# Optimization experiments

Measured on AMD Instinct MI355X. Metric: run time of the kernel, lower is better.

## Reference

```python
import jax, jax.numpy as jnp
import numpy as np

N = 50000      # nodes
E = 800000     # edges (before self loops)
D = 128        # input_dim == hidden_dim == out_channels
H = 1          # heads
L = 3          # layers
SLOPE = 0.2    # GATv2 leaky_relu negative slope


def setup_inputs() -> dict:
    key = jax.random.key(0)
    ks = jax.random.split(key, 9)
    x = jax.random.normal(ks[0], (N, D), dtype=jnp.float32)
    edge_index = jax.random.randint(ks[1], (2, E), 0, N, dtype=jnp.int32)
    s = 1.0 / np.sqrt(D).astype(np.float32)
    # stacked per-layer GATv2Conv params (all layers are D -> H*D here)
    Wl = jax.random.normal(ks[2], (L, D, H * D), dtype=jnp.float32) * s   # lin_l weights
    bl = jnp.zeros((L, H * D), dtype=jnp.float32)
    Wr = jax.random.normal(ks[3], (L, D, H * D), dtype=jnp.float32) * s   # lin_r weights
    br = jnp.zeros((L, H * D), dtype=jnp.float32)
    att = jax.random.normal(ks[4], (L, H, D), dtype=jnp.float32) * s      # attention vector
    bias = jnp.zeros((L, H * D), dtype=jnp.float32)                       # conv output bias
    return {"x": x, "edge_index": edge_index, "Wl": Wl, "bl": bl,
            "Wr": Wr, "br": br, "att": att, "bias": bias}


def reference(x, edge_index, Wl, bl, Wr, br, att, bias):
    # add self loops (PyG GATv2Conv default)
    loops = jnp.arange(N, dtype=edge_index.dtype)
    src = jnp.concatenate([edge_index[0], loops])  # [E+N] message sources j
    dst = jnp.concatenate([edge_index[1], loops])  # [E+N] message targets i

    h = x
    for l in range(L):
        xl = (h @ Wl[l] + bl[l]).reshape(N, H, D)   # source transform
        xr = (h @ Wr[l] + br[l]).reshape(N, H, D)   # target transform
        # edge-wise GATv2 score: att . leaky_relu(xl_j + xr_i)
        e = jax.nn.leaky_relu(xl[src] + xr[dst], SLOPE)      # [E+N, H, D]
        score = jnp.einsum('ehd,hd->eh', e, att[l])          # [E+N, H]
        # segment softmax over incoming edges of each dst node
        m = jax.ops.segment_max(score, dst, num_segments=N)  # [N, H]
        p = jnp.exp(score - m[dst])
        denom = jax.ops.segment_sum(p, dst, num_segments=N)
        alpha = p / (denom[dst] + 1e-16)                     # [E+N, H]
        # weighted scatter-aggregate of source features
        msg = xl[src] * alpha[:, :, None]                    # [E+N, H, D]
        h = jax.ops.segment_sum(msg, dst, num_segments=N).reshape(N, H * D) + bias[l]
        h = jax.nn.relu(h)
    return jax.nn.log_softmax(h, axis=1)
```

## Files before the change

kernel.cpp:

```cpp
#include <hip/hip_runtime.h>
#include <cstdint>
#include <cstddef>

#define N_NODES 50000
#define N_EDGES 800000
#define ET (N_EDGES + N_NODES)
#define D 128
#define NLAYERS 3
#define SLOPE 0.2f
#define NB_SCAN ((N_NODES + 1023) / 1024)

typedef __bf16 bf16x8 __attribute__((ext_vector_type(8)));
typedef float  f32x4  __attribute__((ext_vector_type(4)));
typedef float  f32x2  __attribute__((ext_vector_type(2)));

__device__ __forceinline__ unsigned short f2bf_rne(float v) {
    unsigned u = __float_as_uint(v);
    u += 0x7fffu + ((u >> 16) & 1u);
    return (unsigned short)(u >> 16);
}
__device__ __forceinline__ float bf2f(unsigned short h) {
    return __uint_as_float(((unsigned)h) << 16);
}
__device__ __forceinline__ f32x2 unpack_bf2(unsigned u) {
    f32x2 r;
    r.x = __uint_as_float(u << 16);
    r.y = __uint_as_float(u & 0xffff0000u);
    return r;
}

__global__ void prep_kernel(const float* __restrict__ x,
                            const float* __restrict__ Wl,
                            const float* __restrict__ Wr,
                            const int* __restrict__ dstp,
                            unsigned short* __restrict__ hhi,
                            unsigned short* __restrict__ hlo,
                            unsigned short* __restrict__ wlh,
                            unsigned short* __restrict__ wll,
                            unsigned short* __restrict__ wrh,
                            int* __restrict__ deg)
{
    int idx = blockIdx.x * blockDim.x + threadIdx.x;
    if (idx < (N_NODES * D) / 4) {
        float4 v = ((const float4*)x)[idx];
        unsigned short h0 = f2bf_rne(v.x), h1 = f2bf_rne(v.y);
        unsigned short h2 = f2bf_rne(v.z), h3 = f2bf_rne(v.w);
        unsigned short l0 = f2bf_rne(v.x - bf2f(h0)), l1 = f2bf_rne(v.y - bf2f(h1));
        unsigned short l2 = f2bf_rne(v.z - bf2f(h2)), l3 = f2bf_rne(v.w - bf2f(h3));
        uint2 hw, lw;
        hw.x = (unsigned)h0 | ((unsigned)h1 << 16);
        hw.y = (unsigned)h2 | ((unsigned)h3 << 16);
        lw.x = (unsigned)l0 | ((unsigned)l1 << 16);
        lw.y = (unsigned)l2 | ((unsigned)l3 << 16);
        ((uint2*)hhi)[idx] = hw;
        ((uint2*)hlo)[idx] = lw;
    }
    if (idx < NLAYERS * D * D) {
        int l   = idx / (D * D);
        int rem = idx - l * D * D;
        int kk  = rem / D;
        int nn  = rem - kk * D;
        int tp  = l * D * D + nn * D + kk;
        float v = Wl[idx];
        unsigned short h = f2bf_rne(v);
        wlh[tp] = h;
        wll[tp] = f2bf_rne(v - bf2f(h));
        wrh[tp] = f2bf_rne(Wr[idx]);
    }
    if (idx < ET) {
        int dt = (idx < N_EDGES) ? dstp[idx] : idx - N_EDGES;
        atomicAdd(deg + dt, 1);
    }
}

__global__ void scan1_kernel(const int* __restrict__ deg,
                             int* __restrict__ incl, int* __restrict__ bsum)
{
    __shared__ int tmp[1024];
    int tid = threadIdx.x;
    int i = blockIdx.x * 1024 + tid;
    int v = (i < N_NODES) ? deg[i] : 0;
    tmp[tid] = v;
    __syncthreads();
    #pragma unroll
    for (int o = 1; o < 1024; o <<= 1) {
        int t = (tid >= o) ? tmp[tid - o] : 0;
        __syncthreads();
        tmp[tid] += t;
        __syncthreads();
    }
    if (i < N_NODES) incl[i] = tmp[tid];
    if (tid == 1023) bsum[blockIdx.x] = tmp[1023];
}

__global__ void scan3_kernel(const int* __restrict__ deg, const int* __restrict__ incl,
                             const int* __restrict__ bsum,
                             int* __restrict__ off, int* __restrict__ cursor)
{
    __shared__ int sb[NB_SCAN + 1];
    int tid = threadIdx.x;
    if (tid < 64) {
        int v = (tid < NB_SCAN) ? bsum[tid] : 0;
        int orig = v;
        #pragma unroll
        for (int o = 1; o < 64; o <<= 1) {
            int t = __shfl_up(v, o, 64);
            if (tid >= o) v += t;
        }
        if (tid < NB_SCAN) sb[tid] = v - orig;
        if (tid == 63)     sb[NB_SCAN] = v;
    }
    __syncthreads();
    int i = blockIdx.x * blockDim.x + tid;
    if (i < N_NODES) {
        int e = incl[i] - deg[i] + sb[i >> 10];
        off[i] = e;
        cursor[i] = e;
    } else if (i == N_NODES) {
        off[N_NODES] = sb[NB_SCAN];
    }
}

__global__ void scatter_kernel(const int* __restrict__ srcp, const int* __restrict__ dstp,
                               int* __restrict__ cursor, int* __restrict__ esrc)
{
    int e = blockIdx.x * blockDim.x + threadIdx.x;
    if (e >= ET) return;
    int s, dt;
    if (e < N_EDGES) { s = srcp[e]; dt = dstp[e]; }
    else             { s = e - N_EDGES; dt = s; }
    int pos = atomicAdd(cursor + dt, 1);
    esrc[pos] = s;
}

__global__ __launch_bounds__(256, 2)
void gemm_mfma_kernel(const unsigned short* __restrict__ hhi,
                      const unsigned short* __restrict__ hlo,
                      const unsigned short* __restrict__ wlh,
                      const unsigned short* __restrict__ wll,
                      const unsigned short* __restrict__ wrh,
                      const float* __restrict__ bl, const float* __restrict__ br,
                      unsigned short* __restrict__ xlb, unsigned short* __restrict__ xrb,
                      int n)
{
    int lane = threadIdx.x & 63;
    int wid  = threadIdx.x >> 6;
    int rowB = blockIdx.x >> 1;
    int c0   = (blockIdx.x & 1) * 64;
    int m0   = (rowB * 4 + wid) * 32;
    if (m0 >= n) return;
    int gl = lane & 15;
    int kg = lane >> 4;

    float blc[4], brc[4];
    #pragma unroll
    for (int t = 0; t < 4; t++) {
        blc[t] = bl[c0 + t * 16 + gl];
        brc[t] = br[c0 + t * 16 + gl];
    }

    int ar0 = m0 + gl;      if (ar0 >= n) ar0 = n - 1;
    int ar1 = m0 + 16 + gl; if (ar1 >= n) ar1 = n - 1;
    const unsigned short* ah0 = hhi + (size_t)ar0 * D + kg * 8;
    const unsigned short* al0 = hlo + (size_t)ar0 * D + kg * 8;
    const unsigned short* ah1 = hhi + (size_t)ar1 * D + kg * 8;
    const unsigned short* al1 = hlo + (size_t)ar1 * D + kg * 8;

    f32x4 accl[2][4], accr[2][4];
    #pragma unroll
    for (int rt = 0; rt < 2; rt++)
        #pragma unroll
        for (int t = 0; t < 4; t++) {
            accl[rt][t] = (f32x4){0.f, 0.f, 0.f, 0.f};
            accr[rt][t] = (f32x4){0.f, 0.f, 0.f, 0.f};
        }

    #pragma unroll
    for (int ks = 0; ks < 4; ks++) {
        bf16x8 aH0 = *(const bf16x8*)(ah0 + ks * 32);
        bf16x8 aL0 = *(const bf16x8*)(al0 + ks * 32);
        bf16x8 aH1 = *(const bf16x8*)(ah1 + ks * 32);
        bf16x8 aL1 = *(const bf16x8*)(al1 + ks * 32);
        #pragma unroll
        for (int t = 0; t < 4; t++) {
            size_t boff = (size_t)(c0 + t * 16 + gl) * D + kg * 8 + ks * 32;
            bf16x8 bLH = *(const bf16x8*)(wlh + boff);
            bf16x8 bLL = *(const bf16x8*)(wll + boff);
            bf16x8 bRH = *(const bf16x8*)(wrh + boff);
            accl[0][t] = __builtin_amdgcn_mfma_f32_16x16x32_bf16(aH0, bLH, accl[0][t], 0, 0, 0);
            accl[0][t] = __builtin_amdgcn_mfma_f32_16x16x32_bf16(aL0, bLH, accl[0][t], 0, 0, 0);
            accl[0][t] = __builtin_amdgcn_mfma_f32_16x16x32_bf16(aH0, bLL, accl[0][t], 0, 0, 0);
            accr[0][t] = __builtin_amdgcn_mfma_f32_16x16x32_bf16(aH0, bRH, accr[0][t], 0, 0, 0);
            accl[1][t] = __builtin_amdgcn_mfma_f32_16x16x32_bf16(aH1, bLH, accl[1][t], 0, 0, 0);
            accl[1][t] = __builtin_amdgcn_mfma_f32_16x16x32_bf16(aL1, bLH, accl[1][t], 0, 0, 0);
            accl[1][t] = __builtin_amdgcn_mfma_f32_16x16x32_bf16(aH1, bLL, accl[1][t], 0, 0, 0);
            accr[1][t] = __builtin_amdgcn_mfma_f32_16x16x32_bf16(aH1, bRH, accr[1][t], 0, 0, 0);
        }
    }

    #pragma unroll
    for (int rt = 0; rt < 2; rt++) {
        #pragma unroll
        for (int t = 0; t < 4; t++) {
            int col = c0 + t * 16 + gl;
            #pragma unroll
            for (int r = 0; r < 4; r++) {
                int row = m0 + rt * 16 + kg * 4 + r;
                if (row < n) {
                    xlb[(size_t)row * D + col] = f2bf_rne(accl[rt][t][r] + blc[t]);
                    xrb[(size_t)row * D + col] = f2bf_rne(accr[rt][t][r] + brc[t]);
                }
            }
        }
    }
}

template <int LAST>
__global__ void node_attn_kernel(const unsigned short* __restrict__ xlb,
                                 const unsigned short* __restrict__ xrb,
                                 const float* __restrict__ att,
                                 const float* __restrict__ bias,
                                 const int* __restrict__ off,
                                 const int* __restrict__ esrc,
                                 float* __restrict__ outF,
                                 unsigned short* __restrict__ hhi,
                                 unsigned short* __restrict__ hlo)
{
    int i    = (int)((blockIdx.x * (size_t)blockDim.x + threadIdx.x) >> 6);
    int lane = threadIdx.x & 63;
    if (i >= N_NODES) return;
    int g  = lane >> 4;
    int gl = lane & 15;
    int fb = gl * 8;

    f32x2 aa[4], rr[4];
    {
        float4 a0 = *(const float4*)(att + fb);
        float4 a1 = *(const float4*)(att + fb + 4);
        aa[0] = (f32x2){a0.x, a0.y}; aa[1] = (f32x2){a0.z, a0.w};
        aa[2] = (f32x2){a1.x, a1.y}; aa[3] = (f32x2){a1.z, a1.w};
        uint4 r4 = *(const uint4*)(xrb + (size_t)i * D + fb);
        rr[0] = unpack_bf2(r4.x); rr[1] = unpack_bf2(r4.y);
        rr[2] = unpack_bf2(r4.z); rr[3] = unpack_bf2(r4.w);
    }

    float m = -1e30f, l = 0.f;
    f32x2 acc[4];
    #pragma unroll
    for (int j = 0; j < 4; j++) acc[j] = (f32x2){0.f, 0.f};

    int k    = off[i];
    int kEnd = off[i + 1];

    int kk = k + g;
    bool valid = kk < kEnd;
    int s0 = esrc[valid ? kk : kEnd - 1];
    uint4 x4 = *(const uint4*)(xlb + (size_t)s0 * D + fb);

    while (k < kEnd) {
        int kn = k + 4;
        uint4 nx4 = x4;
        bool nvalid = false;
        if (kn < kEnd) {
            int nkk = kn + g;
            nvalid = nkk < kEnd;
            int ns = esrc[nvalid ? nkk : kEnd - 1];
            nx4 = *(const uint4*)(xlb + (size_t)ns * D + fb);
        }
        f32x2 xx[4];
        xx[0] = unpack_bf2(x4.x); xx[1] = unpack_bf2(x4.y);
        xx[2] = unpack_bf2(x4.z); xx[3] = unpack_bf2(x4.w);
        f32x2 sc2 = {0.f, 0.f};
        #pragma unroll
        for (int j = 0; j < 4; j++) {
            f32x2 v  = xx[j] + rr[j];
            f32x2 lv = __builtin_elementwise_max(v, v * SLOPE);
            sc2 = sc2 + lv * aa[j];
        }
        float sc = sc2.x + sc2.y;
        sc += __shfl_xor(sc, 1, 64);
        sc += __shfl_xor(sc, 2, 64);
        sc += __shfl_xor(sc, 4, 64);
        sc += __shfl_xor(sc, 8, 64);
        if (__any(sc > m + 8.f)) {
            float mn = fmaxf(m, sc);
            float f  = __expf(m - mn);
            float p  = valid ? __expf(sc - mn) : 0.f;
            l = l * f + p;
            f32x2 fv = {f, f}, pv = {p, p};
            #pragma unroll
            for (int j = 0; j < 4; j++) acc[j] = acc[j] * fv + xx[j] * pv;
            m = mn;
        } else {
            float p = valid ? __expf(sc - m) : 0.f;
            l += p;
            f32x2 pv = {p, p};
            #pragma unroll
            for (int j = 0; j < 4; j++) acc[j] = acc[j] + xx[j] * pv;
        }
        x4 = nx4; valid = nvalid;
        k = kn;
    }

    #pragma unroll
    for (int o = 16; o <= 32; o <<= 1) {
        float mo  = __shfl_xor(m, o, 64);
        float lo2 = __shfl_xor(l, o, 64);
        float mn  = fmaxf(m, mo);
        float f1  = __expf(m - mn);
        float f2s = __expf(mo - mn);
        l = l * f1 + lo2 * f2s;
        f32x2 f1v = {f1, f1}, f2v = {f2s, f2s};
        #pragma unroll
        for (int j = 0; j < 4; j++) {
            f32x2 ao;
            ao.x = __shfl_xor(acc[j].x, o, 64);
            ao.y = __shfl_xor(acc[j].y, o, 64);
            acc[j] = acc[j] * f1v + ao * f2v;
        }
        m = mn;
    }

    float inv = 1.f / (l + 1e-16f);
    f32x2 hv[4];
    {
        float4 b0 = *(const float4*)(bias + fb);
        float4 b1 = *(const float4*)(bias + fb + 4);
        f32x2 iv = {inv, inv}, z = {0.f, 0.f};
        f32x2 bb0 = {b0.x, b0.y}, bb1 = {b0.z, b0.w};
        f32x2 bb2 = {b1.x, b1.y}, bb3 = {b1.z, b1.w};
        hv[0] = __builtin_elementwise_max(acc[0] * iv + bb0, z);
        hv[1] = __builtin_elementwise_max(acc[1] * iv + bb1, z);
        hv[2] = __builtin_elementwise_max(acc[2] * iv + bb2, z);
        hv[3] = __builtin_elementwise_max(acc[3] * iv + bb3, z);
    }

    if (LAST) {
        float mx = fmaxf(hv[0].x, hv[0].y);
        #pragma unroll
        for (int j = 1; j < 4; j++) mx = fmaxf(mx, fmaxf(hv[j].x, hv[j].y));
        mx = fmaxf(mx, __shfl_xor(mx, 1, 64));
        mx = fmaxf(mx, __shfl_xor(mx, 2, 64));
        mx = fmaxf(mx, __shfl_xor(mx, 4, 64));
        mx = fmaxf(mx, __shfl_xor(mx, 8, 64));
        float se = 0.f;
        #pragma unroll
        for (int j = 0; j < 4; j++) se += __expf(hv[j].x - mx) + __expf(hv[j].y - mx);
        se += __shfl_xor(se, 1, 64);
        se += __shfl_xor(se, 2, 64);
        se += __shfl_xor(se, 4, 64);
        se += __shfl_xor(se, 8, 64);
        float ls = logf(se) + mx;
        if (g == 0) {
            float4 o0 = make_float4(hv[0].x - ls, hv[0].y - ls, hv[1].x - ls, hv[1].y - ls);
            float4 o1 = make_float4(hv[2].x - ls, hv[2].y - ls, hv[3].x - ls, hv[3].y - ls);
            float* dst = outF + (size_t)i * D + fb;
            *(float4*)(dst)     = o0;
            *(float4*)(dst + 4) = o1;
        }
    } else {
        if (g < 2) {
            unsigned pk[4];
            #pragma unroll
            for (int j = 0; j < 4; j++) {
                float v0 = hv[j].x, v1 = hv[j].y;
                unsigned short h0 = f2bf_rne(v0), h1 = f2bf_rne(v1);
                if (g == 0) pk[j] = (unsigned)h0 | ((unsigned)h1 << 16);
                else {
                    unsigned short l0 = f2bf_rne(v0 - bf2f(h0));
                    unsigned short l1 = f2bf_rne(v1 - bf2f(h1));
                    pk[j] = (unsigned)l0 | ((unsigned)l1 << 16);
                }
            }
            unsigned short* dst = (g == 0 ? hhi : hlo) + (size_t)i * D + fb;
            *(uint4*)dst = make_uint4(pk[0], pk[1], pk[2], pk[3]);
        }
    }
}

extern "C" void kernel_launch(void* const* d_in, const int* in_sizes, int n_in,
                              void* d_out, int out_size, void* d_ws, size_t ws_size,
                              hipStream_t stream)
{
    const float* x    = (const float*)d_in[0];
    const int*   ei   = (const int*)  d_in[1];
    const float* Wl   = (const float*)d_in[2];
    const float* bl   = (const float*)d_in[3];
    const float* Wr   = (const float*)d_in[4];
    const float* br   = (const float*)d_in[5];
    const float* att  = (const float*)d_in[6];
    const float* bias = (const float*)d_in[7];
    float* out = (float*)d_out;

    const int* srcp = ei;
    const int* dstp = ei + N_EDGES;

    const size_t ND = (size_t)N_NODES * D;
    const size_t WSZ = (size_t)NLAYERS * D * D;
    char* ws = (char*)d_ws;
    unsigned short* xlb = (unsigned short*)ws; ws += ND * sizeof(unsigned short);
    unsigned short* xrb = (unsigned short*)ws; ws += ND * sizeof(unsigned short);
    unsigned short* hhi = (unsigned short*)ws; ws += ND * sizeof(unsigned short);
    unsigned short* hlo = (unsigned short*)ws; ws += ND * sizeof(unsigned short);
    unsigned short* wlh = (unsigned short*)ws; ws += WSZ * sizeof(unsigned short);
    unsigned short* wll = (unsigned short*)ws; ws += WSZ * sizeof(unsigned short);
    unsigned short* wrh = (unsigned short*)ws; ws += WSZ * sizeof(unsigned short);
    int* deg    = (int*)ws;  ws += (size_t)N_NODES * sizeof(int);
    int* incl   = (int*)ws;  ws += (size_t)N_NODES * sizeof(int);
    int* off    = (int*)ws;  ws += (size_t)(N_NODES + 1) * sizeof(int);
    int* cursor = (int*)ws;  ws += (size_t)N_NODES * sizeof(int);
    int* bsum   = (int*)ws;  ws += (size_t)NB_SCAN * sizeof(int);
    int* esrc   = (int*)ws;  ws += (size_t)ET * sizeof(int);

    const int prepGrid  = (int)((ND / 4 + 255) / 256);
    const int edgeGrid  = (ET + 255) / 256;
    const int gemmGrid  = ((N_NODES + 127) / 128) * 2;
    const int nodeGrid  = (N_NODES + 3) / 4;
    const int scan3Grid = (N_NODES + 1 + 255) / 256;

    hipMemsetAsync(deg, 0, (size_t)N_NODES * sizeof(int), stream);
    prep_kernel<<<prepGrid, 256, 0, stream>>>(x, Wl, Wr, dstp,
                                              hhi, hlo, wlh, wll, wrh, deg);

    scan1_kernel<<<NB_SCAN, 1024, 0, stream>>>(deg, incl, bsum);
    scan3_kernel<<<scan3Grid, 256, 0, stream>>>(deg, incl, bsum, off, cursor);
    scatter_kernel<<<edgeGrid, 256, 0, stream>>>(srcp, dstp, cursor, esrc);

    for (int l = 0; l < NLAYERS; l++) {
        size_t wOff = (size_t)l * D * D;
        gemm_mfma_kernel<<<gemmGrid, 256, 0, stream>>>(
            hhi, hlo, wlh + wOff, wll + wOff, wrh + wOff,
            bl + (size_t)l * D, br + (size_t)l * D, xlb, xrb, N_NODES);

        if (l == NLAYERS - 1) {
            node_attn_kernel<1><<<nodeGrid, 256, 0, stream>>>(
                xlb, xrb, att + (size_t)l * D, bias + (size_t)l * D,
                off, esrc, out, nullptr, nullptr);
        } else {
            node_attn_kernel<0><<<nodeGrid, 256, 0, stream>>>(
                xlb, xrb, att + (size_t)l * D, bias + (size_t)l * D,
                off, esrc, nullptr, hhi, hlo);
        }
    }
}
```

Baseline: 377.6 us.

## Process two edge groups per attention iteration and shrink GEMM row tiles

The node attention loop now handles eight edges per iteration, two independent groups of four, with double prefetch. This raises memory-level parallelism on the gathered source rows and halves the number of serial softmax-update steps. Separately, the GEMM gives each wave 16 rows instead of 32, preloads the A fragments, raises the launch-bounds occupancy target and doubles the grid. The trade-offs are higher register pressure in the attention kernel and B-fragment loads that are amortised over fewer rows.

```diff
diff --git a/kernel.cpp b/kernel.cpp
--- a/kernel.cpp
+++ b/kernel.cpp
@@ -133,7 +133,7 @@
     esrc[pos] = s;
 }
 
-__global__ __launch_bounds__(256, 2)
+__global__ __launch_bounds__(256, 4)
 void gemm_mfma_kernel(const unsigned short* __restrict__ hhi,
                       const unsigned short* __restrict__ hlo,
                       const unsigned short* __restrict__ wlh,
@@ -147,7 +147,7 @@
     int wid  = threadIdx.x >> 6;
     int rowB = blockIdx.x >> 1;
     int c0   = (blockIdx.x & 1) * 64;
-    int m0   = (rowB * 4 + wid) * 32;
+    int m0   = rowB * 64 + wid * 16;
     if (m0 >= n) return;
     int gl = lane & 15;
     int kg = lane >> 4;
@@ -159,57 +159,47 @@
         brc[t] = br[c0 + t * 16 + gl];
     }
 
-    int ar0 = m0 + gl;      if (ar0 >= n) ar0 = n - 1;
-    int ar1 = m0 + 16 + gl; if (ar1 >= n) ar1 = n - 1;
-    const unsigned short* ah0 = hhi + (size_t)ar0 * D + kg * 8;
-    const unsigned short* al0 = hlo + (size_t)ar0 * D + kg * 8;
-    const unsigned short* ah1 = hhi + (size_t)ar1 * D + kg * 8;
-    const unsigned short* al1 = hlo + (size_t)ar1 * D + kg * 8;
-
-    f32x4 accl[2][4], accr[2][4];
-    #pragma unroll
-    for (int rt = 0; rt < 2; rt++)
-        #pragma unroll
-        for (int t = 0; t < 4; t++) {
-            accl[rt][t] = (f32x4){0.f, 0.f, 0.f, 0.f};
-            accr[rt][t] = (f32x4){0.f, 0.f, 0.f, 0.f};
-        }
-
+    int ar = m0 + gl; if (ar >= n) ar = n - 1;
+    const unsigned short* ah = hhi + (size_t)ar * D + kg * 8;
+    const unsigned short* al = hlo + (size_t)ar * D + kg * 8;
+    bf16x8 Ah[4], Al[4];
     #pragma unroll
     for (int ks = 0; ks < 4; ks++) {
-        bf16x8 aH0 = *(const bf16x8*)(ah0 + ks * 32);
-        bf16x8 aL0 = *(const bf16x8*)(al0 + ks * 32);
-        bf16x8 aH1 = *(const bf16x8*)(ah1 + ks * 32);
-        bf16x8 aL1 = *(const bf16x8*)(al1 + ks * 32);
+        Ah[ks] = *(const bf16x8*)(ah + ks * 32);
+        Al[ks] = *(const bf16x8*)(al + ks * 32);
+    }
+
+    f32x4 accl[4], accr[4];
+    #pragma unroll
+    for (int t = 0; t < 4; t++) {
+        accl[t] = (f32x4){0.f, 0.f, 0.f, 0.f};
+        accr[t] = (f32x4){0.f, 0.f, 0.f, 0.f};
+    }
+
+    #pragma unroll
+    for (int ks = 0; ks < 4; ks++) {
         #pragma unroll
         for (int t = 0; t < 4; t++) {
             size_t boff = (size_t)(c0 + t * 16 + gl) * D + kg * 8 + ks * 32;
             bf16x8 bLH = *(const bf16x8*)(wlh + boff);
             bf16x8 bLL = *(const bf16x8*)(wll + boff);
             bf16x8 bRH = *(const bf16x8*)(wrh + boff);
-            accl[0][t] = __builtin_amdgcn_mfma_f32_16x16x32_bf16(aH0, bLH, accl[0][t], 0, 0, 0);
-            accl[0][t] = __builtin_amdgcn_mfma_f32_16x16x32_bf16(aL0, bLH, accl[0][t], 0, 0, 0);
-            accl[0][t] = __builtin_amdgcn_mfma_f32_16x16x32_bf16(aH0, bLL, accl[0][t], 0, 0, 0);
-            accr[0][t] = __builtin_amdgcn_mfma_f32_16x16x32_bf16(aH0, bRH, accr[0][t], 0, 0, 0);
-            accl[1][t] = __builtin_amdgcn_mfma_f32_16x16x32_bf16(aH1, bLH, accl[1][t], 0, 0, 0);
-            accl[1][t] = __builtin_amdgcn_mfma_f32_16x16x32_bf16(aL1, bLH, accl[1][t], 0, 0, 0);
-            accl[1][t] = __builtin_amdgcn_mfma_f32_16x16x32_bf16(aH1, bLL, accl[1][t], 0, 0, 0);
-            accr[1][t] = __builtin_amdgcn_mfma_f32_16x16x32_bf16(aH1, bRH, accr[1][t], 0, 0, 0);
-        }
-    }
-
-    #pragma unroll
-    for (int rt = 0; rt < 2; rt++) {
-        #pragma unroll
-        for (int t = 0; t < 4; t++) {
-            int col = c0 + t * 16 + gl;
-            #pragma unroll
-            for (int r = 0; r < 4; r++) {
-                int row = m0 + rt * 16 + kg * 4 + r;
-                if (row < n) {
-                    xlb[(size_t)row * D + col] = f2bf_rne(accl[rt][t][r] + blc[t]);
-                    xrb[(size_t)row * D + col] = f2bf_rne(accr[rt][t][r] + brc[t]);
-                }
+            accl[t] = __builtin_amdgcn_mfma_f32_16x16x32_bf16(Ah[ks], bLH, accl[t], 0, 0, 0);
+            accl[t] = __builtin_amdgcn_mfma_f32_16x16x32_bf16(Al[ks], bLH, accl[t], 0, 0, 0);
+            accl[t] = __builtin_amdgcn_mfma_f32_16x16x32_bf16(Ah[ks], bLL, accl[t], 0, 0, 0);
+            accr[t] = __builtin_amdgcn_mfma_f32_16x16x32_bf16(Ah[ks], bRH, accr[t], 0, 0, 0);
+        }
+    }
+
+    #pragma unroll
+    for (int t = 0; t < 4; t++) {
+        int col = c0 + t * 16 + gl;
+        #pragma unroll
+        for (int r = 0; r < 4; r++) {
+            int row = m0 + kg * 4 + r;
+            if (row < n) {
+                xlb[(size_t)row * D + col] = f2bf_rne(accl[t][r] + blc[t]);
+                xrb[(size_t)row * D + col] = f2bf_rne(accr[t][r] + brc[t]);
             }
         }
     }
@@ -251,54 +241,74 @@
 
     int k    = off[i];
     int kEnd = off[i + 1];
-
-    int kk = k + g;
-    bool valid = kk < kEnd;
-    int s0 = esrc[valid ? kk : kEnd - 1];
-    uint4 x4 = *(const uint4*)(xlb + (size_t)s0 * D + fb);
+    int last = kEnd - 1;
+
+    int ka = k + g, kb = k + 4 + g;
+    bool va = ka < kEnd, vb = kb < kEnd;
+    int sa = esrc[va ? ka : last];
+    int sb = esrc[vb ? kb : last];
+    uint4 x4a = *(const uint4*)(xlb + (size_t)sa * D + fb);
+    uint4 x4b = *(const uint4*)(xlb + (size_t)sb * D + fb);
 
     while (k < kEnd) {
-        int kn = k + 4;
-        uint4 nx4 = x4;
-        bool nvalid = false;
+        int kn = k + 8;
+        uint4 nxa = x4a, nxb = x4b;
+        bool nva = false, nvb = false;
         if (kn < kEnd) {
-            int nkk = kn + g;
-            nvalid = nkk < kEnd;
-            int ns = esrc[nvalid ? nkk : kEnd - 1];
-            nx4 = *(const uint4*)(xlb + (size_t)ns * D + fb);
-        }
-        f32x2 xx[4];
-        xx[0] = unpack_bf2(x4.x); xx[1] = unpack_bf2(x4.y);
-        xx[2] = unpack_bf2(x4.z); xx[3] = unpack_bf2(x4.w);
-        f32x2 sc2 = {0.f, 0.f};
+            int nka = kn + g, nkb = kn + 4 + g;
+            nva = nka < kEnd; nvb = nkb < kEnd;
+            int nsa = esrc[nva ? nka : last];
+            int nsb = esrc[nvb ? nkb : last];
+            nxa = *(const uint4*)(xlb + (size_t)nsa * D + fb);
+            nxb = *(const uint4*)(xlb + (size_t)nsb * D + fb);
+        }
+        f32x2 xa[4], xb[4];
+        xa[0] = unpack_bf2(x4a.x); xa[1] = unpack_bf2(x4a.y);
+        xa[2] = unpack_bf2(x4a.z); xa[3] = unpack_bf2(x4a.w);
+        xb[0] = unpack_bf2(x4b.x); xb[1] = unpack_bf2(x4b.y);
+        xb[2] = unpack_bf2(x4b.z); xb[3] = unpack_bf2(x4b.w);
+        f32x2 s2a = {0.f, 0.f}, s2b = {0.f, 0.f};
         #pragma unroll
         for (int j = 0; j < 4; j++) {
-            f32x2 v  = xx[j] + rr[j];
-            f32x2 lv = __builtin_elementwise_max(v, v * SLOPE);
-            sc2 = sc2 + lv * aa[j];
-        }
-        float sc = sc2.x + sc2.y;
-        sc += __shfl_xor(sc, 1, 64);
-        sc += __shfl_xor(sc, 2, 64);
-        sc += __shfl_xor(sc, 4, 64);
-        sc += __shfl_xor(sc, 8, 64);
-        if (__any(sc > m + 8.f)) {
-            float mn = fmaxf(m, sc);
+            f32x2 va_ = xa[j] + rr[j];
+            f32x2 la_ = __builtin_elementwise_max(va_, va_ * SLOPE);
+            s2a = s2a + la_ * aa[j];
+            f32x2 vb_ = xb[j] + rr[j];
+            f32x2 lb_ = __builtin_elementwise_max(vb_, vb_ * SLOPE);
+            s2b = s2b + lb_ * aa[j];
+        }
+        float sca = s2a.x + s2a.y;
+        float scb = s2b.x + s2b.y;
+        sca += __shfl_xor(sca, 1, 64);
+        scb += __shfl_xor(scb, 1, 64);
+        sca += __shfl_xor(sca, 2, 64);
+        scb += __shfl_xor(scb, 2, 64);
+        sca += __shfl_xor(sca, 4, 64);
+        scb += __shfl_xor(scb, 4, 64);
+        sca += __shfl_xor(sca, 8, 64);
+        scb += __shfl_xor(scb, 8, 64);
+        float mx2 = fmaxf(sca, scb);
+        if (__any(mx2 > m + 8.f)) {
+            float mn = fmaxf(m, mx2);
             float f  = __expf(m - mn);
-            float p  = valid ? __expf(sc - mn) : 0.f;
-            l = l * f + p;
-            f32x2 fv = {f, f}, pv = {p, p};
+            float pa = va ? __expf(sca - mn) : 0.f;
+            float pb = vb ? __expf(scb - mn) : 0.f;
+            l = l * f + pa + pb;
+            f32x2 fv = {f, f}, pav = {pa, pa}, pbv = {pb, pb};
             #pragma unroll
-            for (int j = 0; j < 4; j++) acc[j] = acc[j] * fv + xx[j] * pv;
+            for (int j = 0; j < 4; j++)
+                acc[j] = acc[j] * fv + xa[j] * pav + xb[j] * pbv;
             m = mn;
         } else {
-            float p = valid ? __expf(sc - m) : 0.f;
-            l += p;
-            f32x2 pv = {p, p};
+            float pa = va ? __expf(sca - m) : 0.f;
+            float pb = vb ? __expf(scb - m) : 0.f;
+            l += pa + pb;
+            f32x2 pav = {pa, pa}, pbv = {pb, pb};
             #pragma unroll
-            for (int j = 0; j < 4; j++) acc[j] = acc[j] + xx[j] * pv;
-        }
-        x4 = nx4; valid = nvalid;
+            for (int j = 0; j < 4; j++)
+                acc[j] = acc[j] + xa[j] * pav + xb[j] * pbv;
+        }
+        x4a = nxa; x4b = nxb; va = nva; vb = nvb;
         k = kn;
     }
 
@@ -414,7 +424,7 @@
 
     const int prepGrid  = (int)((ND / 4 + 255) / 256);
     const int edgeGrid  = (ET + 255) / 256;
-    const int gemmGrid  = ((N_NODES + 127) / 128) * 2;
+    const int gemmGrid  = ((N_NODES + 63) / 64) * 2;
     const int nodeGrid  = (N_NODES + 3) / 4;
     const int scan3Grid = (N_NODES + 1 + 255) / 256;
 
```

Result: slower. 418.0 us (+10.7%).

## Split GATv2 leaky_relu into linear and abs terms; process two edges per iteration

Applied to the files above, without the earlier changes.

Rewrites leaky_relu(v) as 0.6v + 0.4|v|, so the linear part of the attention score becomes a per-source scalar, computed in the GEMM epilogue via a warp reduction and atomic add. The per-target scalar is computed once per node. The edge loop now handles two edges per lane group with double-buffered prefetch to raise memory-level parallelism. It adds a memset and atomics per layer, plus an extra scalar gather per edge.

```diff
diff --git a/kernel.cpp b/kernel.cpp
--- a/kernel.cpp
+++ b/kernel.cpp
@@ -140,8 +140,9 @@
                       const unsigned short* __restrict__ wll,
                       const unsigned short* __restrict__ wrh,
                       const float* __restrict__ bl, const float* __restrict__ br,
+                      const float* __restrict__ att,
                       unsigned short* __restrict__ xlb, unsigned short* __restrict__ xrb,
-                      int n)
+                      float* __restrict__ bs, int n)
 {
     int lane = threadIdx.x & 63;
     int wid  = threadIdx.x >> 6;
@@ -152,11 +153,12 @@
     int gl = lane & 15;
     int kg = lane >> 4;
 
-    float blc[4], brc[4];
+    float blc[4], brc[4], attc[4];
     #pragma unroll
     for (int t = 0; t < 4; t++) {
-        blc[t] = bl[c0 + t * 16 + gl];
-        brc[t] = br[c0 + t * 16 + gl];
+        blc[t]  = bl [c0 + t * 16 + gl];
+        brc[t]  = br [c0 + t * 16 + gl];
+        attc[t] = att[c0 + t * 16 + gl];
     }
 
     int ar0 = m0 + gl;      if (ar0 >= n) ar0 = n - 1;
@@ -201,15 +203,23 @@
     #pragma unroll
     for (int rt = 0; rt < 2; rt++) {
         #pragma unroll
-        for (int t = 0; t < 4; t++) {
-            int col = c0 + t * 16 + gl;
-            #pragma unroll
-            for (int r = 0; r < 4; r++) {
-                int row = m0 + rt * 16 + kg * 4 + r;
-                if (row < n) {
-                    xlb[(size_t)row * D + col] = f2bf_rne(accl[rt][t][r] + blc[t]);
+        for (int r = 0; r < 4; r++) {
+            int row = m0 + rt * 16 + kg * 4 + r;
+            if (row < n) {
+                float p = 0.f;
+                #pragma unroll
+                for (int t = 0; t < 4; t++) {
+                    int col = c0 + t * 16 + gl;
+                    float vl = accl[rt][t][r] + blc[t];
+                    xlb[(size_t)row * D + col] = f2bf_rne(vl);
                     xrb[(size_t)row * D + col] = f2bf_rne(accr[rt][t][r] + brc[t]);
+                    p = fmaf(attc[t], vl, p);
                 }
+                p += __shfl_xor(p, 1, 64);
+                p += __shfl_xor(p, 2, 64);
+                p += __shfl_xor(p, 4, 64);
+                p += __shfl_xor(p, 8, 64);
+                if (gl == 0) unsafeAtomicAdd(bs + row, 0.6f * p);
             }
         }
     }
@@ -218,6 +228,7 @@
 template <int LAST>
 __global__ void node_attn_kernel(const unsigned short* __restrict__ xlb,
                                  const unsigned short* __restrict__ xrb,
+                                 const float* __restrict__ bs,
                                  const float* __restrict__ att,
                                  const float* __restrict__ bias,
                                  const int* __restrict__ off,
@@ -233,72 +244,110 @@
     int gl = lane & 15;
     int fb = gl * 8;
 
-    f32x2 aa[4], rr[4];
+    float aav[8], rrv[8];
     {
         float4 a0 = *(const float4*)(att + fb);
         float4 a1 = *(const float4*)(att + fb + 4);
-        aa[0] = (f32x2){a0.x, a0.y}; aa[1] = (f32x2){a0.z, a0.w};
-        aa[2] = (f32x2){a1.x, a1.y}; aa[3] = (f32x2){a1.z, a1.w};
+        aav[0] = a0.x; aav[1] = a0.y; aav[2] = a0.z; aav[3] = a0.w;
+        aav[4] = a1.x; aav[5] = a1.y; aav[6] = a1.z; aav[7] = a1.w;
         uint4 r4 = *(const uint4*)(xrb + (size_t)i * D + fb);
-        rr[0] = unpack_bf2(r4.x); rr[1] = unpack_bf2(r4.y);
-        rr[2] = unpack_bf2(r4.z); rr[3] = unpack_bf2(r4.w);
+        f32x2 q;
+        q = unpack_bf2(r4.x); rrv[0] = q.x; rrv[1] = q.y;
+        q = unpack_bf2(r4.y); rrv[2] = q.x; rrv[3] = q.y;
+        q = unpack_bf2(r4.z); rrv[4] = q.x; rrv[5] = q.y;
+        q = unpack_bf2(r4.w); rrv[6] = q.x; rrv[7] = q.y;
+    }
+    float bd;
+    {
+        float pd = 0.f;
+        #pragma unroll
+        for (int j = 0; j < 8; j++) pd = fmaf(aav[j], rrv[j], pd);
+        pd += __shfl_xor(pd, 1, 64);
+        pd += __shfl_xor(pd, 2, 64);
+        pd += __shfl_xor(pd, 4, 64);
+        pd += __shfl_xor(pd, 8, 64);
+        bd = 0.6f * pd;
     }
 
     float m = -1e30f, l = 0.f;
-    f32x2 acc[4];
-    #pragma unroll
-    for (int j = 0; j < 4; j++) acc[j] = (f32x2){0.f, 0.f};
+    float acc[8];
+    #pragma unroll
+    for (int j = 0; j < 8; j++) acc[j] = 0.f;
 
     int k    = off[i];
     int kEnd = off[i + 1];
-
-    int kk = k + g;
-    bool valid = kk < kEnd;
-    int s0 = esrc[valid ? kk : kEnd - 1];
-    uint4 x4 = *(const uint4*)(xlb + (size_t)s0 * D + fb);
+    int last = kEnd - 1;
+
+    int ka = k + g, kb = k + 4 + g;
+    bool va = ka < kEnd, vb = kb < kEnd;
+    int sa = esrc[va ? ka : last];
+    int sb = esrc[vb ? kb : last];
+    uint4 x4a = *(const uint4*)(xlb + (size_t)sa * D + fb);
+    uint4 x4b = *(const uint4*)(xlb + (size_t)sb * D + fb);
+    float bsa = bs[sa], bsb = bs[sb];
 
     while (k < kEnd) {
-        int kn = k + 4;
-        uint4 nx4 = x4;
-        bool nvalid = false;
+        int kn = k + 8;
+        uint4 nxa = x4a, nxb = x4b;
+        float nbsa = bsa, nbsb = bsb;
+        bool nva = false, nvb = false;
         if (kn < kEnd) {
-            int nkk = kn + g;
-            nvalid = nkk < kEnd;
-            int ns = esrc[nvalid ? nkk : kEnd - 1];
-            nx4 = *(const uint4*)(xlb + (size_t)ns * D + fb);
-        }
-        f32x2 xx[4];
-        xx[0] = unpack_bf2(x4.x); xx[1] = unpack_bf2(x4.y);
-        xx[2] = unpack_bf2(x4.z); xx[3] = unpack_bf2(x4.w);
-        f32x2 sc2 = {0.f, 0.f};
-        #pragma unroll
-        for (int j = 0; j < 4; j++) {
-            f32x2 v  = xx[j] + rr[j];
-            f32x2 lv = __builtin_elementwise_max(v, v * SLOPE);
-            sc2 = sc2 + lv * aa[j];
-        }
-        float sc = sc2.x + sc2.y;
-        sc += __shfl_xor(sc, 1, 64);
-        sc += __shfl_xor(sc, 2, 64);
-        sc += __shfl_xor(sc, 4, 64);
-        sc += __shfl_xor(sc, 8, 64);
-        if (__any(sc > m + 8.f)) {
-            float mn = fmaxf(m, sc);
+            int nka = kn + g, nkb = kn + 4 + g;
+            nva = nka < kEnd; nvb = nkb < kEnd;
+            int nsa = esrc[nva ? nka : last];
+            int nsb = esrc[nvb ? nkb : last];
+            nxa = *(const uint4*)(xlb + (size_t)nsa * D + fb);
+            nxb = *(const uint4*)(xlb + (size_t)nsb * D + fb);
+            nbsa = bs[nsa]; nbsb = bs[nsb];
+        }
+        float xa[8], xb[8];
+        {
+            f32x2 q;
+            q = unpack_bf2(x4a.x); xa[0] = q.x; xa[1] = q.y;
+            q = unpack_bf2(x4a.y); xa[2] = q.x; xa[3] = q.y;
+            q = unpack_bf2(x4a.z); xa[4] = q.x; xa[5] = q.y;
+            q = unpack_bf2(x4a.w); xa[6] = q.x; xa[7] = q.y;
+            q = unpack_bf2(x4b.x); xb[0] = q.x; xb[1] = q.y;
+            q = unpack_bf2(x4b.y); xb[2] = q.x; xb[3] = q.y;
+            q = unpack_bf2(x4b.z); xb[4] = q.x; xb[5] = q.y;
+            q = unpack_bf2(x4b.w); xb[6] = q.x; xb[7] = q.y;
+        }
+        float s2a = 0.f, s2b = 0.f;
+        #pragma unroll
+        for (int j = 0; j < 8; j++) {
+            s2a = fmaf(aav[j], fabsf(xa[j] + rrv[j]), s2a);
+            s2b = fmaf(aav[j], fabsf(xb[j] + rrv[j]), s2b);
+        }
+        s2a += __shfl_xor(s2a, 1, 64);
+        s2b += __shfl_xor(s2b, 1, 64);
+        s2a += __shfl_xor(s2a, 2, 64);
+        s2b += __shfl_xor(s2b, 2, 64);
+        s2a += __shfl_xor(s2a, 4, 64);
+        s2b += __shfl_xor(s2b, 4, 64);
+        s2a += __shfl_xor(s2a, 8, 64);
+        s2b += __shfl_xor(s2b, 8, 64);
+        float sca = bsa + bd + 0.4f * s2a;
+        float scb = bsb + bd + 0.4f * s2b;
+        float mx2 = fmaxf(sca, scb);
+        if (__any(mx2 > m + 8.f)) {
+            float mn = fmaxf(m, mx2);
             float f  = __expf(m - mn);
-            float p  = valid ? __expf(sc - mn) : 0.f;
-            l = l * f + p;
-            f32x2 fv = {f, f}, pv = {p, p};
+            float pa = va ? __expf(sca - mn) : 0.f;
+            float pb = vb ? __expf(scb - mn) : 0.f;
+            l = l * f + pa + pb;
             #pragma unroll
-            for (int j = 0; j < 4; j++) acc[j] = acc[j] * fv + xx[j] * pv;
+            for (int j = 0; j < 8; j++)
+                acc[j] = fmaf(acc[j], f, fmaf(xa[j], pa, xb[j] * pb));
             m = mn;
         } else {
-            float p = valid ? __expf(sc - m) : 0.f;
-            l += p;
-            f32x2 pv = {p, p};
+            float pa = va ? __expf(sca - m) : 0.f;
+            float pb = vb ? __expf(scb - m) : 0.f;
+            l += pa + pb;
             #pragma unroll
-            for (int j = 0; j < 4; j++) acc[j] = acc[j] + xx[j] * pv;
-        }
-        x4 = nx4; valid = nvalid;
+            for (int j = 0; j < 8; j++)
+                acc[j] = fmaf(xa[j], pa, fmaf(xb[j], pb, acc[j]));
+        }
+        x4a = nxa; x4b = nxb; bsa = nbsa; bsb = nbsb; va = nva; vb = nvb;
         k = kn;
     }
 
@@ -310,50 +359,43 @@
         float f1  = __expf(m - mn);
         float f2s = __expf(mo - mn);
         l = l * f1 + lo2 * f2s;
-        f32x2 f1v = {f1, f1}, f2v = {f2s, f2s};
-        #pragma unroll
-        for (int j = 0; j < 4; j++) {
-            f32x2 ao;
-            ao.x = __shfl_xor(acc[j].x, o, 64);
-            ao.y = __shfl_xor(acc[j].y, o, 64);
-            acc[j] = acc[j] * f1v + ao * f2v;
+        #pragma unroll
+        for (int j = 0; j < 8; j++) {
+            float ao = __shfl_xor(acc[j], o, 64);
+            acc[j] = acc[j] * f1 + ao * f2s;
         }
         m = mn;
     }
 
     float inv = 1.f / (l + 1e-16f);
-    f32x2 hv[4];
+    float hv[8];
     {
         float4 b0 = *(const float4*)(bias + fb);
         float4 b1 = *(const float4*)(bias + fb + 4);
-        f32x2 iv = {inv, inv}, z = {0.f, 0.f};
-        f32x2 bb0 = {b0.x, b0.y}, bb1 = {b0.z, b0.w};
-        f32x2 bb2 = {b1.x, b1.y}, bb3 = {b1.z, b1.w};
-        hv[0] = __builtin_elementwise_max(acc[0] * iv + bb0, z);
-        hv[1] = __builtin_elementwise_max(acc[1] * iv + bb1, z);
-        hv[2] = __builtin_elementwise_max(acc[2] * iv + bb2, z);
-        hv[3] = __builtin_elementwise_max(acc[3] * iv + bb3, z);
+        float bb[8] = {b0.x, b0.y, b0.z, b0.w, b1.x, b1.y, b1.z, b1.w};
+        #pragma unroll
+        for (int j = 0; j < 8; j++) hv[j] = fmaxf(fmaf(acc[j], inv, bb[j]), 0.f);
     }
 
     if (LAST) {
-        float mx = fmaxf(hv[0].x, hv[0].y);
-        #pragma unroll
-        for (int j = 1; j < 4; j++) mx = fmaxf(mx, fmaxf(hv[j].x, hv[j].y));
+        float mx = hv[0];
+        #pragma unroll
+        for (int j = 1; j < 8; j++) mx = fmaxf(mx, hv[j]);
         mx = fmaxf(mx, __shfl_xor(mx, 1, 64));
         mx = fmaxf(mx, __shfl_xor(mx, 2, 64));
         mx = fmaxf(mx, __shfl_xor(mx, 4, 64));
         mx = fmaxf(mx, __shfl_xor(mx, 8, 64));
         float se = 0.f;
         #pragma unroll
-        for (int j = 0; j < 4; j++) se += __expf(hv[j].x - mx) + __expf(hv[j].y - mx);
+        for (int j = 0; j < 8; j++) se += __expf(hv[j] - mx);
         se += __shfl_xor(se, 1, 64);
         se += __shfl_xor(se, 2, 64);
         se += __shfl_xor(se, 4, 64);
         se += __shfl_xor(se, 8, 64);
         float ls = logf(se) + mx;
         if (g == 0) {
-            float4 o0 = make_float4(hv[0].x - ls, hv[0].y - ls, hv[1].x - ls, hv[1].y - ls);
-            float4 o1 = make_float4(hv[2].x - ls, hv[2].y - ls, hv[3].x - ls, hv[3].y - ls);
+            float4 o0 = make_float4(hv[0] - ls, hv[1] - ls, hv[2] - ls, hv[3] - ls);
+            float4 o1 = make_float4(hv[4] - ls, hv[5] - ls, hv[6] - ls, hv[7] - ls);
             float* dst = outF + (size_t)i * D + fb;
             *(float4*)(dst)     = o0;
             *(float4*)(dst + 4) = o1;
@@ -363,7 +405,7 @@
             unsigned pk[4];
             #pragma unroll
             for (int j = 0; j < 4; j++) {
-                float v0 = hv[j].x, v1 = hv[j].y;
+                float v0 = hv[j * 2], v1 = hv[j * 2 + 1];
                 unsigned short h0 = f2bf_rne(v0), h1 = f2bf_rne(v1);
                 if (g == 0) pk[j] = (unsigned)h0 | ((unsigned)h1 << 16);
                 else {
@@ -405,6 +447,7 @@
     unsigned short* wlh = (unsigned short*)ws; ws += WSZ * sizeof(unsigned short);
     unsigned short* wll = (unsigned short*)ws; ws += WSZ * sizeof(unsigned short);
     unsigned short* wrh = (unsigned short*)ws; ws += WSZ * sizeof(unsigned short);
+    float* bs   = (float*)ws; ws += (size_t)N_NODES * sizeof(float);
     int* deg    = (int*)ws;  ws += (size_t)N_NODES * sizeof(int);
     int* incl   = (int*)ws;  ws += (size_t)N_NODES * sizeof(int);
     int* off    = (int*)ws;  ws += (size_t)(N_NODES + 1) * sizeof(int);
@@ -428,17 +471,19 @@
 
     for (int l = 0; l < NLAYERS; l++) {
         size_t wOff = (size_t)l * D * D;
+        hipMemsetAsync(bs, 0, (size_t)N_NODES * sizeof(float), stream);
         gemm_mfma_kernel<<<gemmGrid, 256, 0, stream>>>(
             hhi, hlo, wlh + wOff, wll + wOff, wrh + wOff,
-            bl + (size_t)l * D, br + (size_t)l * D, xlb, xrb, N_NODES);
+            bl + (size_t)l * D, br + (size_t)l * D, att + (size_t)l * D,
+            xlb, xrb, bs, N_NODES);
 
         if (l == NLAYERS - 1) {
             node_attn_kernel<1><<<nodeGrid, 256, 0, stream>>>(
-                xlb, xrb, att + (size_t)l * D, bias + (size_t)l * D,
+                xlb, xrb, bs, att + (size_t)l * D, bias + (size_t)l * D,
                 off, esrc, out, nullptr, nullptr);
         } else {
             node_attn_kernel<0><<<nodeGrid, 256, 0, stream>>>(
-                xlb, xrb, att + (size_t)l * D, bias + (size_t)l * D,
+                xlb, xrb, bs, att + (size_t)l * D, bias + (size_t)l * D,
                 off, esrc, nullptr, hhi, hlo);
         }
     }
```

Result: no change. 381.3 us (+1.0%).
